# Kernel tuning notes

Hardware: AMD Instinct MI355X
Metric: run time of the kernel (lower is better)

Reference implementation:

```python
import jax, jax.numpy as jnp
import numpy as np

N = 100000
E = 3200000
F_IN = 27
H1, C1 = 8, 8
H2, C2 = 1, 2
NEG_SLOPE = 0.2


def gat_conv(x, src, dst, W, a_src, a_dst, b, heads, ch, n_nodes):
    # x: [N, F_in]; src/dst: [E'] (self-loops already appended)
    h = (x @ W).reshape(n_nodes, heads, ch)            # [N, H, C]
    alpha_src = jnp.sum(h * a_src, axis=-1)            # [N, H]
    alpha_dst = jnp.sum(h * a_dst, axis=-1)            # [N, H]
    e = jax.nn.leaky_relu(alpha_src[src] + alpha_dst[dst], NEG_SLOPE)  # [E', H]
    m = jax.ops.segment_max(e, dst, num_segments=n_nodes)             # [N, H]
    ex = jnp.exp(e - m[dst])
    denom = jax.ops.segment_sum(ex, dst, num_segments=n_nodes)        # [N, H]
    alpha = ex / denom[dst]                                           # [E', H]
    out = jax.ops.segment_sum(h[src] * alpha[:, :, None], dst, num_segments=n_nodes)
    return out.reshape(n_nodes, heads * ch) + b


def setup_inputs() -> dict:
    key = jax.random.key(0)
    ks = jax.random.split(key, 10)
    x = jax.random.normal(ks[0], (N, F_IN), dtype=jnp.float32)
    edge_index = jax.random.randint(ks[1], (2, E), 0, N, dtype=jnp.int64)
    s1 = 1.0 / np.sqrt(F_IN)
    s2 = 1.0 / np.sqrt(H1 * C1)
    W1 = jax.random.uniform(ks[2], (F_IN, H1 * C1), jnp.float32, -s1, s1)
    a_src1 = jax.random.uniform(ks[3], (H1, C1), jnp.float32, -s1, s1)
    a_dst1 = jax.random.uniform(ks[4], (H1, C1), jnp.float32, -s1, s1)
    b1 = jnp.zeros((H1 * C1,), jnp.float32)
    W2 = jax.random.uniform(ks[5], (H1 * C1, H2 * C2), jnp.float32, -s2, s2)
    a_src2 = jax.random.uniform(ks[6], (H2, C2), jnp.float32, -s2, s2)
    a_dst2 = jax.random.uniform(ks[7], (H2, C2), jnp.float32, -s2, s2)
    b2 = jnp.zeros((H2 * C2,), jnp.float32)
    return {"x": x, "edge_index": edge_index, "W1": W1, "a_src1": a_src1,
            "a_dst1": a_dst1, "b1": b1, "W2": W2, "a_src2": a_src2,
            "a_dst2": a_dst2, "b2": b2}


def reference(x, edge_index, W1, a_src1, a_dst1, b1, W2, a_src2, a_dst2, b2):
    # eval mode: dropouts are identity. PyG GATConv adds self-loops by default.
    loop = jnp.arange(N, dtype=edge_index.dtype)
    src = jnp.concatenate([edge_index[0], loop])
    dst = jnp.concatenate([edge_index[1], loop])
    h = jax.nn.elu(gat_conv(x, src, dst, W1, a_src1, a_dst1, b1, H1, C1, N))
    out = gat_conv(h, src, dst, W2, a_src2, a_dst2, b2, H2, C2, N)
    return jax.nn.log_softmax(out, axis=1)
```

## Files before the change

### kernel.cpp

```cpp
#include <hip/hip_runtime.h>
#include <hip/hip_fp16.h>
#include <math.h>

#define NN 100000
#define EE 3200000
#define ET (EE + NN)

#define H1n 8
#define C1n 8
#define F1n 64
#define FINn 27
#define NEG 0.2f

#define NPB 128
#define NB 782
#define STRIDE 5120
#define TILE 4096
#define ABLK 256
#define WIN (STRIDE + NPB)
#define FBLK 512

typedef float floatx2 __attribute__((ext_vector_type(2)));

static __device__ __forceinline__ float lrelu(float v) {
    return v > 0.f ? v : NEG * v;
}

__global__ __launch_bounds__(ABLK) void k_binA(const int* __restrict__ ei,
                                               int* __restrict__ tail,
                                               int* __restrict__ recs) {
    __shared__ int hist[NB];
    __shared__ int lofs[NB];
    __shared__ int cur[NB];
    __shared__ int gpos[NB];
    __shared__ int sorted[TILE];
    __shared__ unsigned short sbkt[TILE];
    __shared__ int part[ABLK];

    int tid = threadIdx.x;
    long long e0 = (long long)blockIdx.x * TILE;
    int cnt = (int)min((long long)TILE, (long long)EE - e0);

    for (int i = tid; i < NB; i += ABLK) hist[i] = 0;
    __syncthreads();

    int ss[TILE / ABLK], dd[TILE / ABLK];
    #pragma unroll
    for (int k = 0; k < TILE / ABLK; ++k) {
        int idx = k * ABLK + tid;
        if (idx < cnt) {
            ss[k] = ei[e0 + idx];
            dd[k] = ei[EE + e0 + idx];
            atomicAdd(&hist[dd[k] >> 7], 1);
        }
    }
    __syncthreads();
    {
        const int CH = (NB + ABLK - 1) / ABLK;
        int beg = tid * CH, end = min(beg + CH, NB);
        int s = 0;
        for (int i = beg; i < end; ++i) s += hist[i];
        part[tid] = s;
        __syncthreads();
        for (int off = 1; off < ABLK; off <<= 1) {
            int add = (tid >= off) ? part[tid - off] : 0;
            __syncthreads();
            part[tid] += add;
            __syncthreads();
        }
        int ex = (tid > 0) ? part[tid - 1] : 0;
        for (int i = beg; i < end; ++i) {
            lofs[i] = ex;
            cur[i] = ex;
            ex += hist[i];
        }
    }
    __syncthreads();
    #pragma unroll
    for (int k = 0; k < TILE / ABLK; ++k) {
        int idx = k * ABLK + tid;
        if (idx < cnt) {
            int b = dd[k] >> 7;
            int r = atomicAdd(&cur[b], 1);
            sorted[r] = ss[k] | ((dd[k] & (NPB - 1)) << 17);
            sbkt[r] = (unsigned short)b;
        }
    }
    __syncthreads();
    for (int i = tid; i < NB; i += ABLK) {
        int c = hist[i];
        if (c > 0) gpos[i] = atomicAdd(&tail[i], c);
    }
    __syncthreads();
    for (int t = tid; t < cnt; t += ABLK) {
        int b = sbkt[t];
        recs[(size_t)b * STRIDE + gpos[b] + (t - lofs[b])] = sorted[t];
    }
}

__global__ __launch_bounds__(256) void k_h1(const float* __restrict__ x,
                                            const float* __restrict__ W1,
                                            const float* __restrict__ a_src1,
                                            const float* __restrict__ a_dst1,
                                            unsigned char* __restrict__ h1q,
                                            __half* __restrict__ as1h,
                                            float* __restrict__ ad1) {
    int gt = blockIdx.x * blockDim.x + threadIdx.x;
    int n = gt >> 6;
    if (n >= NN) return;
    int lane = threadIdx.x & 63;
    const float* xr = x + (size_t)n * FINn;
    float s = 0.f;
    #pragma unroll
    for (int k = 0; k < FINn; ++k) s = fmaf(xr[k], W1[k * F1n + lane], s);
    float s2 = __shfl_down(s, 1, 64);
    if (!(lane & 1)) {
        int pk = __builtin_amdgcn_cvt_pk_fp8_f32(s, s2, 0, false);
        ((unsigned short*)(h1q + (size_t)n * F1n))[lane >> 1] =
            (unsigned short)(pk & 0xFFFF);
    }
    float ps = s * a_src1[lane];
    float pd = s * a_dst1[lane];
    #pragma unroll
    for (int off = 1; off < 8; off <<= 1) {
        ps += __shfl_xor(ps, off, 64);
        pd += __shfl_xor(pd, off, 64);
    }
    if ((lane & 7) == 0) {
        int h = lane >> 3;
        as1h[n * H1n + h] = __float2half(ps);
        ad1[n * H1n + h] = pd;
    }
}

__global__ __launch_bounds__(FBLK) void k_f1(const int* __restrict__ recs,
                                             const int* __restrict__ tail,
                                             const unsigned* __restrict__ h1q,
                                             const __half* __restrict__ as1h,
                                             const float* __restrict__ ad1,
                                             const float* __restrict__ b1,
                                             const float* __restrict__ W2,
                                             const float* __restrict__ a_src2,
                                             const float* __restrict__ a_dst2,
                                             uint2* __restrict__ rec2) {
    __shared__ int hist[NPB];
    __shared__ int cur[NPB];
    __shared__ int rloc[NPB + 1];
    __shared__ int window[WIN];
    __shared__ int wtot[2];

    int b = blockIdx.x;
    int tid = threadIdx.x;
    int node0 = b * NPB;
    int nodes = min(NPB, NN - node0);
    int rcnt = tail[b];
    const int* rb = recs + (size_t)b * STRIDE;

    if (tid < NPB) hist[tid] = 0;
    __syncthreads();
    for (int i = tid; i < rcnt; i += FBLK) atomicAdd(&hist[rb[i] >> 17], 1);
    __syncthreads();
    int v = 0, inc = 0;
    if (tid < NPB) {
        v = (tid < nodes) ? hist[tid] + 1 : 0;
        inc = v;
        #pragma unroll
        for (int off = 1; off < 64; off <<= 1) {
            int t = __shfl_up(inc, off, 64);
            if ((tid & 63) >= off) inc += t;
        }
        if ((tid & 63) == 63) wtot[tid >> 6] = inc;
    }
    __syncthreads();
    if (tid < NPB) {
        if (tid >= 64) inc += wtot[0];
        int ex = inc - v;
        if (tid < nodes) {
            rloc[tid] = ex;
            cur[tid] = ex + 1;
            window[ex] = node0 + tid;
        }
    }
    if (tid == 0) rloc[nodes] = wtot[0] + wtot[1];
    __syncthreads();
    for (int i = tid; i < rcnt; i += FBLK) {
        int r = rb[i];
        int p = atomicAdd(&cur[r >> 17], 1);
        window[p] = r & 0x1FFFF;
    }
    __syncthreads();

    int lane = tid & 63;
    int wv = tid >> 6;
    int e8 = lane >> 3;
    int hh = lane & 7;
    int q = lane >> 4;
    int c4 = lane & 15;
    int bpe = e8 << 2;
    int bpq = q << 2;
    int bpx = ((q << 3) + (c4 >> 1)) << 2;

    for (int ln = wv; ln < nodes; ln += FBLK / 64) {
        int n = node0 + ln;
        float adh = ad1[(n << 3) + hh];
        int beg = rloc[ln], end = rloc[ln + 1];
        float a0 = 0.f, a1 = 0.f, a2 = 0.f, a3 = 0.f, den = 0.f;

        for (int base = beg; base < end; base += 64) {
            int cnt = min(64, end - base);
            int sidx = (lane < cnt) ? window[base + lane] : 0;
            for (int sb = 0; sb < cnt; sb += 8) {
                int sb4 = sb << 2;
                int s_sc = __builtin_amdgcn_ds_bpermute(sb4 + bpe, sidx);
                float A = __half2float(as1h[((unsigned)s_sc << 3) + hh]);
                float sc = A + adh;
                sc = fmaxf(sc, 0.2f * sc);
                float x = (sb + e8 < cnt) ? __expf(sc) : 0.f;
                den += x;
                int xi = __float_as_int(x);
                #pragma unroll
                for (int jj = 0; jj < 2; ++jj) {
                    int s_a = __builtin_amdgcn_ds_bpermute(sb4 + (jj << 4) + bpq, sidx);
                    int xr_ = __builtin_amdgcn_ds_bpermute((jj << 7) + bpx, xi);
                    float xv = __int_as_float(xr_);
                    unsigned dw = h1q[((unsigned)s_a << 4) + c4];
                    floatx2 lo = __builtin_amdgcn_cvt_pk_f32_fp8((int)dw, false);
                    floatx2 hi = __builtin_amdgcn_cvt_pk_f32_fp8((int)dw, true);
                    a0 = fmaf(xv, lo.x, a0);
                    a1 = fmaf(xv, lo.y, a1);
                    a2 = fmaf(xv, hi.x, a2);
                    a3 = fmaf(xv, hi.y, a3);
                }
            }
        }

        den += __shfl_xor(den, 8, 64);
        den += __shfl_xor(den, 16, 64);
        den += __shfl_xor(den, 32, 64);
        den = __int_as_float(
            __builtin_amdgcn_ds_bpermute((c4 >> 1) << 2, __float_as_int(den)));
        #pragma unroll
        for (int off = 16; off < 64; off <<= 1) {
            a0 += __shfl_xor(a0, off, 64);
            a1 += __shfl_xor(a1, off, 64);
            a2 += __shfl_xor(a2, off, 64);
            a3 += __shfl_xor(a3, off, 64);
        }
        float inv = 1.f / den;
        float v0 = a0 * inv + b1[c4 * 4 + 0];
        float v1 = a1 * inv + b1[c4 * 4 + 1];
        float v2 = a2 * inv + b1[c4 * 4 + 2];
        float v3 = a3 * inv + b1[c4 * 4 + 3];
        v0 = v0 > 0.f ? v0 : expm1f(v0);
        v1 = v1 > 0.f ? v1 : expm1f(v1);
        v2 = v2 > 0.f ? v2 : expm1f(v2);
        v3 = v3 > 0.f ? v3 : expm1f(v3);
        float p0 = v0 * W2[(c4 * 4 + 0) * 2 + 0] + v1 * W2[(c4 * 4 + 1) * 2 + 0] +
                   v2 * W2[(c4 * 4 + 2) * 2 + 0] + v3 * W2[(c4 * 4 + 3) * 2 + 0];
        float p1 = v0 * W2[(c4 * 4 + 0) * 2 + 1] + v1 * W2[(c4 * 4 + 1) * 2 + 1] +
                   v2 * W2[(c4 * 4 + 2) * 2 + 1] + v3 * W2[(c4 * 4 + 3) * 2 + 1];
        #pragma unroll
        for (int off = 1; off < 16; off <<= 1) {
            p0 += __shfl_xor(p0, off, 64);
            p1 += __shfl_xor(p1, off, 64);
        }
        if (lane == 0) {
            float as2 = p0 * a_src2[0] + p1 * a_src2[1];
            float ad2 = p0 * a_dst2[0] + p1 * a_dst2[1];
            __half2 lo2 = __floats2half2_rn(p0, p1);
            __half2 hi2 = __floats2half2_rn(as2, ad2);
            uint2 r;
            r.x = *(unsigned*)&lo2;
            r.y = *(unsigned*)&hi2;
            rec2[n] = r;
        }
    }
}

__global__ __launch_bounds__(FBLK) void k_f2(const int* __restrict__ recs,
                                             const int* __restrict__ tail,
                                             const uint2* __restrict__ rec2,
                                             const float* __restrict__ b2,
                                             float* __restrict__ out) {
    __shared__ int hist[NPB];
    __shared__ int cur[NPB];
    __shared__ int rloc[NPB + 1];
    __shared__ int window[WIN];
    __shared__ int wtot[2];

    int b = blockIdx.x;
    int tid = threadIdx.x;
    int node0 = b * NPB;
    int nodes = min(NPB, NN - node0);
    int rcnt = tail[b];
    const int* rb = recs + (size_t)b * STRIDE;

    if (tid < NPB) hist[tid] = 0;
    __syncthreads();
    for (int i = tid; i < rcnt; i += FBLK) atomicAdd(&hist[rb[i] >> 17], 1);
    __syncthreads();
    int v = 0, inc = 0;
    if (tid < NPB) {
        v = (tid < nodes) ? hist[tid] + 1 : 0;
        inc = v;
        #pragma unroll
        for (int off = 1; off < 64; off <<= 1) {
            int t = __shfl_up(inc, off, 64);
            if ((tid & 63) >= off) inc += t;
        }
        if ((tid & 63) == 63) wtot[tid >> 6] = inc;
    }
    __syncthreads();
    if (tid < NPB) {
        if (tid >= 64) inc += wtot[0];
        int ex = inc - v;
        if (tid < nodes) {
            rloc[tid] = ex;
            cur[tid] = ex + 1;
            window[ex] = node0 + tid;
        }
    }
    if (tid == 0) rloc[nodes] = wtot[0] + wtot[1];
    __syncthreads();
    for (int i = tid; i < rcnt; i += FBLK) {
        int r = rb[i];
        int p = atomicAdd(&cur[r >> 17], 1);
        window[p] = r & 0x1FFFF;
    }
    __syncthreads();

    int lane = tid & 63;
    int wv = tid >> 6;
    for (int ln = wv; ln < nodes; ln += FBLK / 64) {
        int n = node0 + ln;
        __half2 mysd = *(const __half2*)&rec2[n].y;
        float adv = __half2float(__high2half(mysd));
        int beg = rloc[ln], end = rloc[ln + 1];
        float den = 0.f, a0 = 0.f, a1 = 0.f;
        for (int i = beg + lane; i < end; i += 64) {
            int s = window[i];
            uint2 rv = rec2[s];
            __half2 h01 = *(const __half2*)&rv.x;
            __half2 hsd = *(const __half2*)&rv.y;
            float e = lrelu(__half2float(__low2half(hsd)) + adv);
            float ex = __expf(e);
            den += ex;
            a0 = fmaf(ex, __half2float(__low2half(h01)), a0);
            a1 = fmaf(ex, __half2float(__high2half(h01)), a1);
        }
        #pragma unroll
        for (int off = 32; off > 0; off >>= 1) {
            den += __shfl_xor(den, off, 64);
            a0 += __shfl_xor(a0, off, 64);
            a1 += __shfl_xor(a1, off, 64);
        }
        if (lane == 0) {
            float v0 = a0 / den + b2[0];
            float v1 = a1 / den + b2[1];
            float mx = fmaxf(v0, v1);
            float ls = mx + logf(__expf(v0 - mx) + __expf(v1 - mx));
            out[n * 2 + 0] = v0 - ls;
            out[n * 2 + 1] = v1 - ls;
        }
    }
}

extern "C" void kernel_launch(void* const* d_in, const int* in_sizes, int n_in,
                              void* d_out, int out_size, void* d_ws, size_t ws_size,
                              hipStream_t stream) {
    const float* x      = (const float*)d_in[0];
    const int*   ei     = (const int*)d_in[1];
    const float* W1     = (const float*)d_in[2];
    const float* a_src1 = (const float*)d_in[3];
    const float* a_dst1 = (const float*)d_in[4];
    const float* b1     = (const float*)d_in[5];
    const float* W2     = (const float*)d_in[6];
    const float* a_src2 = (const float*)d_in[7];
    const float* a_dst2 = (const float*)d_in[8];
    const float* b2     = (const float*)d_in[9];
    float* out = (float*)d_out;

    char* wsb = (char*)d_ws;
    size_t o = 0;
    uint2* rec2 = (uint2*)wsb;                   o += (size_t)NN * 8;
    #define ALLOC(name, type, count) type* name = (type*)(wsb + o); o += (size_t)(count) * 4;
    ALLOC(ad1,    float, NN * H1n)
    ALLOC(recs,   int,   (size_t)NB * STRIDE)
    ALLOC(tail,   int,   NB)
    #undef ALLOC
    __half* as1h = (__half*)(wsb + o);               o += (size_t)NN * H1n * 2;
    unsigned char* h1q = (unsigned char*)(wsb + o);  o += (size_t)NN * F1n;

    const int B = 256;
    #define GRID(n) ((unsigned)(((long long)(n) + B - 1) / B))

    hipMemsetAsync(tail, 0, (size_t)NB * sizeof(int), stream);
    k_binA<<<(EE + TILE - 1) / TILE, ABLK, 0, stream>>>(ei, tail, recs);

    k_h1<<<GRID((size_t)NN * 64), B, 0, stream>>>(x, W1, a_src1, a_dst1, h1q, as1h, ad1);

    k_f1<<<NB, FBLK, 0, stream>>>(recs, tail, (const unsigned*)h1q, as1h, ad1, b1,
                                  W2, a_src2, a_dst2, rec2);

    k_f2<<<NB, FBLK, 0, stream>>>(recs, tail, rec2, b2, out);
    #undef GRID
}
```

Measured before the change: 218.2 us.

## Fuse edge binning with layer-1 projection and use shared atomics in layer 2

Merges the edge-binning kernel and the per-node layer-1 projection into one launch, with blocks past the binning range doing the projection. This removes a launch and lets the two independent jobs overlap. Layer 2 drops the per-block local counting sort and instead accumulates exp-weighted sums per destination node with LDS float atomics, adding the self-loop term at the end. Nontemporal loads are added for the streamed edge records. The LDS atomics can contend on high-degree nodes, and float atomic ordering makes the summation order nondeterministic.

Result: slower. 247.3 us (+13.4%).

```diff
diff --git a/kernel.cpp b/kernel.cpp
--- a/kernel.cpp
+++ b/kernel.cpp
@@ -20,15 +20,25 @@
 #define WIN (STRIDE + NPB)
 #define FBLK 512
 
+#define ABLOCKS ((EE + TILE - 1) / TILE)
+#define H1BLOCKS ((NN * 64) / 256)
+
 typedef float floatx2 __attribute__((ext_vector_type(2)));
 
 static __device__ __forceinline__ float lrelu(float v) {
     return v > 0.f ? v : NEG * v;
 }
 
-__global__ __launch_bounds__(ABLK) void k_binA(const int* __restrict__ ei,
-                                               int* __restrict__ tail,
-                                               int* __restrict__ recs) {
+__global__ __launch_bounds__(ABLK) void k_binA_h1(const int* __restrict__ ei,
+                                                  int* __restrict__ tail,
+                                                  int* __restrict__ recs,
+                                                  const float* __restrict__ x,
+                                                  const float* __restrict__ W1,
+                                                  const float* __restrict__ a_src1,
+                                                  const float* __restrict__ a_dst1,
+                                                  unsigned char* __restrict__ h1q,
+                                                  __half* __restrict__ as1h,
+                                                  float* __restrict__ ad1) {
     __shared__ int hist[NB];
     __shared__ int lofs[NB];
     __shared__ int cur[NB];
@@ -38,6 +48,37 @@
     __shared__ int part[ABLK];
 
     int tid = threadIdx.x;
+
+    if (blockIdx.x >= ABLOCKS) {
+        int gt = (blockIdx.x - ABLOCKS) * ABLK + tid;
+        int n = gt >> 6;
+        if (n >= NN) return;
+        int lane = tid & 63;
+        const float* xr = x + (size_t)n * FINn;
+        float s = 0.f;
+        #pragma unroll
+        for (int k = 0; k < FINn; ++k) s = fmaf(xr[k], W1[k * F1n + lane], s);
+        float s2 = __shfl_down(s, 1, 64);
+        if (!(lane & 1)) {
+            int pk = __builtin_amdgcn_cvt_pk_fp8_f32(s, s2, 0, false);
+            ((unsigned short*)(h1q + (size_t)n * F1n))[lane >> 1] =
+                (unsigned short)(pk & 0xFFFF);
+        }
+        float ps = s * a_src1[lane];
+        float pd = s * a_dst1[lane];
+        #pragma unroll
+        for (int off = 1; off < 8; off <<= 1) {
+            ps += __shfl_xor(ps, off, 64);
+            pd += __shfl_xor(pd, off, 64);
+        }
+        if ((lane & 7) == 0) {
+            int h = lane >> 3;
+            as1h[n * H1n + h] = __float2half(ps);
+            ad1[n * H1n + h] = pd;
+        }
+        return;
+    }
+
     long long e0 = (long long)blockIdx.x * TILE;
     int cnt = (int)min((long long)TILE, (long long)EE - e0);
 
@@ -49,8 +90,8 @@
     for (int k = 0; k < TILE / ABLK; ++k) {
         int idx = k * ABLK + tid;
         if (idx < cnt) {
-            ss[k] = ei[e0 + idx];
-            dd[k] = ei[EE + e0 + idx];
+            ss[k] = __builtin_nontemporal_load(&ei[e0 + idx]);
+            dd[k] = __builtin_nontemporal_load(&ei[EE + e0 + idx]);
             atomicAdd(&hist[dd[k] >> 7], 1);
         }
     }
@@ -95,41 +136,6 @@
     for (int t = tid; t < cnt; t += ABLK) {
         int b = sbkt[t];
         recs[(size_t)b * STRIDE + gpos[b] + (t - lofs[b])] = sorted[t];
-    }
-}
-
-__global__ __launch_bounds__(256) void k_h1(const float* __restrict__ x,
-                                            const float* __restrict__ W1,
-                                            const float* __restrict__ a_src1,
-                                            const float* __restrict__ a_dst1,
-                                            unsigned char* __restrict__ h1q,
-                                            __half* __restrict__ as1h,
-                                            float* __restrict__ ad1) {
-    int gt = blockIdx.x * blockDim.x + threadIdx.x;
-    int n = gt >> 6;
-    if (n >= NN) return;
-    int lane = threadIdx.x & 63;
-    const float* xr = x + (size_t)n * FINn;
-    float s = 0.f;
-    #pragma unroll
-    for (int k = 0; k < FINn; ++k) s = fmaf(xr[k], W1[k * F1n + lane], s);
-    float s2 = __shfl_down(s, 1, 64);
-    if (!(lane & 1)) {
-        int pk = __builtin_amdgcn_cvt_pk_fp8_f32(s, s2, 0, false);
-        ((unsigned short*)(h1q + (size_t)n * F1n))[lane >> 1] =
-            (unsigned short)(pk & 0xFFFF);
-    }
-    float ps = s * a_src1[lane];
-    float pd = s * a_dst1[lane];
-    #pragma unroll
-    for (int off = 1; off < 8; off <<= 1) {
-        ps += __shfl_xor(ps, off, 64);
-        pd += __shfl_xor(pd, off, 64);
-    }
-    if ((lane & 7) == 0) {
-        int h = lane >> 3;
-        as1h[n * H1n + h] = __float2half(ps);
-        ad1[n * H1n + h] = pd;
     }
 }
 
@@ -158,7 +164,8 @@
 
     if (tid < NPB) hist[tid] = 0;
     __syncthreads();
-    for (int i = tid; i < rcnt; i += FBLK) atomicAdd(&hist[rb[i] >> 17], 1);
+    for (int i = tid; i < rcnt; i += FBLK)
+        atomicAdd(&hist[__builtin_nontemporal_load(&rb[i]) >> 17], 1);
     __syncthreads();
     int v = 0, inc = 0;
     if (tid < NPB) {
@@ -184,7 +191,7 @@
     if (tid == 0) rloc[nodes] = wtot[0] + wtot[1];
     __syncthreads();
     for (int i = tid; i < rcnt; i += FBLK) {
-        int r = rb[i];
+        int r = __builtin_nontemporal_load(&rb[i]);
         int p = atomicAdd(&cur[r >> 17], 1);
         window[p] = r & 0x1FFFF;
     }
@@ -282,11 +289,8 @@
                                              const uint2* __restrict__ rec2,
                                              const float* __restrict__ b2,
                                              float* __restrict__ out) {
-    __shared__ int hist[NPB];
-    __shared__ int cur[NPB];
-    __shared__ int rloc[NPB + 1];
-    __shared__ int window[WIN];
-    __shared__ int wtot[2];
+    __shared__ float accd[NPB], acc0[NPB], acc1[NPB];
+    __shared__ uint2 myrec[NPB];
 
     int b = blockIdx.x;
     int tid = threadIdx.x;
@@ -295,73 +299,49 @@
     int rcnt = tail[b];
     const int* rb = recs + (size_t)b * STRIDE;
 
-    if (tid < NPB) hist[tid] = 0;
-    __syncthreads();
-    for (int i = tid; i < rcnt; i += FBLK) atomicAdd(&hist[rb[i] >> 17], 1);
-    __syncthreads();
-    int v = 0, inc = 0;
     if (tid < NPB) {
-        v = (tid < nodes) ? hist[tid] + 1 : 0;
-        inc = v;
-        #pragma unroll
-        for (int off = 1; off < 64; off <<= 1) {
-            int t = __shfl_up(inc, off, 64);
-            if ((tid & 63) >= off) inc += t;
-        }
-        if ((tid & 63) == 63) wtot[tid >> 6] = inc;
-    }
-    __syncthreads();
-    if (tid < NPB) {
-        if (tid >= 64) inc += wtot[0];
-        int ex = inc - v;
-        if (tid < nodes) {
-            rloc[tid] = ex;
-            cur[tid] = ex + 1;
-            window[ex] = node0 + tid;
-        }
-    }
-    if (tid == 0) rloc[nodes] = wtot[0] + wtot[1];
-    __syncthreads();
+        accd[tid] = 0.f;
+        acc0[tid] = 0.f;
+        acc1[tid] = 0.f;
+        myrec[tid] = rec2[node0 + min(tid, nodes - 1)];
+    }
+    __syncthreads();
+
     for (int i = tid; i < rcnt; i += FBLK) {
-        int r = rb[i];
-        int p = atomicAdd(&cur[r >> 17], 1);
-        window[p] = r & 0x1FFFF;
-    }
-    __syncthreads();
-
-    int lane = tid & 63;
-    int wv = tid >> 6;
-    for (int ln = wv; ln < nodes; ln += FBLK / 64) {
-        int n = node0 + ln;
-        __half2 mysd = *(const __half2*)&rec2[n].y;
-        float adv = __half2float(__high2half(mysd));
-        int beg = rloc[ln], end = rloc[ln + 1];
-        float den = 0.f, a0 = 0.f, a1 = 0.f;
-        for (int i = beg + lane; i < end; i += 64) {
-            int s = window[i];
-            uint2 rv = rec2[s];
-            __half2 h01 = *(const __half2*)&rv.x;
-            __half2 hsd = *(const __half2*)&rv.y;
-            float e = lrelu(__half2float(__low2half(hsd)) + adv);
-            float ex = __expf(e);
-            den += ex;
-            a0 = fmaf(ex, __half2float(__low2half(h01)), a0);
-            a1 = fmaf(ex, __half2float(__high2half(h01)), a1);
-        }
-        #pragma unroll
-        for (int off = 32; off > 0; off >>= 1) {
-            den += __shfl_xor(den, off, 64);
-            a0 += __shfl_xor(a0, off, 64);
-            a1 += __shfl_xor(a1, off, 64);
-        }
-        if (lane == 0) {
-            float v0 = a0 / den + b2[0];
-            float v1 = a1 / den + b2[1];
-            float mx = fmaxf(v0, v1);
-            float ls = mx + logf(__expf(v0 - mx) + __expf(v1 - mx));
-            out[n * 2 + 0] = v0 - ls;
-            out[n * 2 + 1] = v1 - ls;
-        }
+        int r = __builtin_nontemporal_load(&rb[i]);
+        int s = r & 0x1FFFF;
+        int dL = r >> 17;
+        uint2 rv = rec2[s];
+        __half2 ssd = *(const __half2*)&rv.y;
+        __half2 dsd = *(const __half2*)&myrec[dL].y;
+        float e = lrelu(__half2float(__low2half(ssd)) +
+                        __half2float(__high2half(dsd)));
+        float ex = __expf(e);
+        __half2 h01 = *(const __half2*)&rv.x;
+        atomicAdd(&accd[dL], ex);
+        atomicAdd(&acc0[dL], ex * __half2float(__low2half(h01)));
+        atomicAdd(&acc1[dL], ex * __half2float(__high2half(h01)));
+    }
+    __syncthreads();
+
+    if (tid < nodes) {
+        uint2 rv = myrec[tid];
+        __half2 h01 = *(const __half2*)&rv.x;
+        __half2 hsd = *(const __half2*)&rv.y;
+        float e = lrelu(__half2float(__low2half(hsd)) +
+                        __half2float(__high2half(hsd)));
+        float ex = __expf(e);
+        float den = accd[tid] + ex;
+        float a0 = acc0[tid] + ex * __half2float(__low2half(h01));
+        float a1 = acc1[tid] + ex * __half2float(__high2half(h01));
+        float v0 = a0 / den + b2[0];
+        float v1 = a1 / den + b2[1];
+        float mx = fmaxf(v0, v1);
+        float ls = mx + logf(__expf(v0 - mx) + __expf(v1 - mx));
+        float2 o;
+        o.x = v0 - ls;
+        o.y = v1 - ls;
+        ((float2*)out)[node0 + tid] = o;
     }
 }
 
@@ -391,17 +371,13 @@
     __half* as1h = (__half*)(wsb + o);               o += (size_t)NN * H1n * 2;
     unsigned char* h1q = (unsigned char*)(wsb + o);  o += (size_t)NN * F1n;
 
-    const int B = 256;
-    #define GRID(n) ((unsigned)(((long long)(n) + B - 1) / B))
-
     hipMemsetAsync(tail, 0, (size_t)NB * sizeof(int), stream);
-    k_binA<<<(EE + TILE - 1) / TILE, ABLK, 0, stream>>>(ei, tail, recs);
-
-    k_h1<<<GRID((size_t)NN * 64), B, 0, stream>>>(x, W1, a_src1, a_dst1, h1q, as1h, ad1);
+    k_binA_h1<<<ABLOCKS + H1BLOCKS, ABLK, 0, stream>>>(ei, tail, recs,
+                                                       x, W1, a_src1, a_dst1,
+                                                       h1q, as1h, ad1);
 
     k_f1<<<NB, FBLK, 0, stream>>>(recs, tail, (const unsigned*)h1q, as1h, ad1, b1,
                                   W2, a_src2, a_dst2, rec2);
 
     k_f2<<<NB, FBLK, 0, stream>>>(recs, tail, rec2, b2, out);
-    #undef GRID
-}
+}
```
